# Kernel tuning notes

Measured on AMD Instinct MI355X. Metric: run time of the kernel, lower is better.

## Reference

```python
import jax, jax.numpy as jnp
import numpy as np

L, H, F, FH, MLPD = 12, 12, 768, 64, 3072  # layers, heads, d_model, head_dim, mlp hidden
GH, GW = 32, 32
N = 1 + GH * GW  # cls token + patches
EPS = 1e-6
QK_SCALE = FH ** (-0.5)
STAGE_ENDS = (2, 5, 8, 11)  # last layer index of each of the 4 stages (3 layers/stage)


def _relpos_index(h, w):
    # standard timm BEiT relative position index with 3 extra cls entries
    coords = np.stack(np.meshgrid(np.arange(h), np.arange(w), indexing="ij"))  # 2,h,w
    cf = coords.reshape(2, -1)
    rel = (cf[:, :, None] - cf[:, None, :]).transpose(1, 2, 0).astype(np.int64)  # hw,hw,2
    rel[:, :, 0] += h - 1
    rel[:, :, 1] += w - 1
    rel[:, :, 0] *= 2 * w - 1
    num_rel = (2 * h - 1) * (2 * w - 1) + 3
    idx = np.zeros((h * w + 1, h * w + 1), dtype=np.int32)
    idx[1:, 1:] = rel.sum(-1)
    idx[0, 0:] = num_rel - 3
    idx[0:, 0] = num_rel - 2
    idx[0, 0] = num_rel - 1
    return idx, num_rel


def setup_inputs() -> dict:
    key = jax.random.key(0)
    ks = jax.random.split(key, 10)
    s = 0.02
    idx, R = _relpos_index(GH, GW)
    return dict(
        patch_tokens=jax.random.normal(ks[0], (1, GH * GW, F), jnp.float32),
        cls_token=jax.random.normal(ks[1], (1, 1, F), jnp.float32) * s,
        ln1_w=jnp.ones((L, F), jnp.float32),
        ln1_b=jnp.zeros((L, F), jnp.float32),
        qkv_w=jax.random.normal(ks[2], (L, 3 * F, F), jnp.float32) * s,
        q_bias=jax.random.normal(ks[3], (L, H, FH), jnp.float32) * s,
        v_bias=jax.random.normal(ks[4], (L, H, FH), jnp.float32) * s,
        proj_w=jax.random.normal(ks[5], (L, F, F), jnp.float32) * s,
        proj_b=jnp.zeros((L, F), jnp.float32),
        scale_attn=jnp.full((L, F), 0.1, jnp.float32),
        ln2_w=jnp.ones((L, F), jnp.float32),
        ln2_b=jnp.zeros((L, F), jnp.float32),
        fc1_w=jax.random.normal(ks[6], (L, MLPD, F), jnp.float32) * s,
        fc1_b=jnp.zeros((L, MLPD), jnp.float32),
        fc2_w=jax.random.normal(ks[7], (L, F, MLPD), jnp.float32) * s,
        fc2_b=jnp.zeros((L, F), jnp.float32),
        scale_mlp=jnp.full((L, F), 0.1, jnp.float32),
        relpos_table=jax.random.normal(ks[8], (L, R, H), jnp.float32) * s,
        relpos_index=jnp.asarray(idx),
        patch_grid_hw=jnp.array([GH, GW], jnp.int32),
    )


def _ln(x, w, b):
    mu = jnp.mean(x, -1, keepdims=True)
    var = jnp.mean(jnp.square(x - mu), -1, keepdims=True)
    return (x - mu) * jax.lax.rsqrt(var + EPS) * w + b


def reference(patch_tokens, cls_token, ln1_w, ln1_b, qkv_w, q_bias, v_bias,
              proj_w, proj_b, scale_attn, ln2_w, ln2_b, fc1_w, fc1_b, fc2_w,
              fc2_b, scale_mlp, relpos_table, relpos_index, patch_grid_hw):
    B = patch_tokens.shape[0]
    tokens = jnp.concatenate(
        [jnp.broadcast_to(cls_token, (B, 1, F)), patch_tokens], axis=1)  # B,N,F

    params = dict(ln1_w=ln1_w, ln1_b=ln1_b, qkv_w=qkv_w, q_bias=q_bias,
                  v_bias=v_bias, proj_w=proj_w, proj_b=proj_b,
                  scale_attn=scale_attn, ln2_w=ln2_w, ln2_b=ln2_b,
                  fc1_w=fc1_w, fc1_b=fc1_b, fc2_w=fc2_w, fc2_b=fc2_b,
                  scale_mlp=scale_mlp, relpos_table=relpos_table)

    def step(x, p):
        h = _ln(x, p['ln1_w'], p['ln1_b'])
        qkv = jnp.einsum('bnf,gf->bng', h, p['qkv_w'])          # B,N,3F (no bias)
        qkv = qkv.reshape(B, N, 3, H, FH).transpose(2, 0, 3, 1, 4)
        q, k, v = qkv[0], qkv[1], qkv[2]                         # B,H,N,fh
        q = (q + p['q_bias'][None, :, None, :]) * QK_SCALE
        v = v + p['v_bias'][None, :, None, :]
        bias = p['relpos_table'][relpos_index]                   # N,N,H
        attn = jnp.einsum('bhnd,bhmd->bhnm', q, k) + bias.transpose(2, 0, 1)[None]
        w = jax.nn.softmax(attn, axis=-1)
        o = jnp.einsum('bhnm,bhmd->bhnd', w, v).transpose(0, 2, 1, 3).reshape(B, N, F)
        o = o @ p['proj_w'].T + p['proj_b']
        x = x + p['scale_attn'] * o
        h2 = _ln(x, p['ln2_w'], p['ln2_b'])
        m = jax.nn.gelu(h2 @ p['fc1_w'].T + p['fc1_b'], approximate=False)
        m = m @ p['fc2_w'].T + p['fc2_b']
        x = x + p['scale_mlp'] * m
        return x, x

    _, ys = jax.lax.scan(step, tokens, params)  # ys: L,B,N,F
    return (ys[STAGE_ENDS[0]], ys[STAGE_ENDS[1]], ys[STAGE_ENDS[2]], ys[STAGE_ENDS[3]])
```

## Files before the change

### kernel.cpp

```cpp
#include <hip/hip_runtime.h>
#include <hip/hip_bf16.h>
#include <math.h>

#define L_LAYERS 12
#define H_HEADS  12
#define F_DIM    768
#define FH_DIM   64
#define MLPD     3072
#define NT       1025
#define NTP      1056
#define THREE_F  2304
#define R_REL    3972
#define QK_SCALE 0.125f
#define QB       64
#define KB       128

#define CQKV  (THREE_F * F_DIM)
#define CPROJ (F_DIM * F_DIM)
#define CFC1  (MLPD * F_DIM)
#define CFC2  (F_DIM * MLPD)

typedef short short8_t __attribute__((ext_vector_type(8)));
typedef float f32x4_t  __attribute__((ext_vector_type(4)));
typedef __attribute__((address_space(1))) const void* gptr_t;
typedef __attribute__((address_space(3))) void*       lptr_t;

typedef __hip_bfloat16 bf16;

static __device__ inline unsigned short f2bf(float f) {
    __hip_bfloat16 b(f);
    unsigned short u;
    __builtin_memcpy(&u, &b, 2);
    return u;
}

__device__ inline void xcd_remap(int& tx, int& ty) {
    int gx = gridDim.x, gy = gridDim.y;
    int b = blockIdx.y * gx + blockIdx.x;
    int total = gx * gy;
    int q = total >> 3, r = total & 7;
    int xcd = b & 7, i = b >> 3;
    int pos = (xcd < r) ? xcd * (q + 1) + i : r * (q + 1) + (xcd - r) * q + i;
    ty = pos / gx;
    tx = pos - ty * gx;
}

__global__ void init_x_k(const float* __restrict__ patch, const float* __restrict__ cls,
                         float* __restrict__ x) {
    int i = blockIdx.x * 256 + threadIdx.x;
    if (i >= NT * F_DIM) return;
    int n = i / F_DIM, f = i - n * F_DIM;
    x[i] = (n == 0) ? cls[f] : patch[(size_t)(n - 1) * F_DIM + f];
}

__global__ void zero_vt_k(bf16* __restrict__ vt) {
    int i = blockIdx.x * 256 + threadIdx.x;
    int total = H_HEADS * FH_DIM * NTP;
    #pragma unroll
    for (int j = 0; j < 8; ++j) {
        int e = i * 8 + j;
        if (e < total) vt[e] = __hip_bfloat16(0.0f);
    }
}

__global__ void rp16_k(const int* __restrict__ rp, unsigned short* __restrict__ rp16) {
    int i = blockIdx.x * 256 + threadIdx.x;
    if (i < NT * NT) rp16[i] = (unsigned short)rp[i];
}

__global__ void tableT_k(const float* __restrict__ t, float* __restrict__ tt) {
    int i = blockIdx.x * 256 + threadIdx.x;
    if (i >= L_LAYERS * R_REL * H_HEADS) return;
    int l = i / (R_REL * H_HEADS), rem = i - l * (R_REL * H_HEADS);
    int rr = rem / H_HEADS, hh = rem - rr * H_HEADS;
    tt[((size_t)l * H_HEADS + hh) * R_REL + rr] = t[i];
}

__global__ void conv_all_k(const float* __restrict__ qkv_w, const float* __restrict__ proj_w,
                           const float* __restrict__ fc1_w, const float* __restrict__ fc2_w,
                           bf16* __restrict__ wq, bf16* __restrict__ wp,
                           bf16* __restrict__ w1, bf16* __restrict__ w2) {
    const long A1 = (long)L_LAYERS * CQKV;
    const long A2 = A1 + (long)L_LAYERS * CPROJ;
    const long A3 = A2 + (long)L_LAYERS * CFC1;
    const long A4 = A3 + (long)L_LAYERS * CFC2;
    const long total4 = A4 >> 2;
    for (long qd = (long)blockIdx.x * 256 + threadIdx.x; qd < total4;
         qd += (long)gridDim.x * 256) {
        long e = qd << 2;
        const float* s; bf16* d; long off;
        if (e < A1)      { s = qkv_w;  d = wq; off = e; }
        else if (e < A2) { s = proj_w; d = wp; off = e - A1; }
        else if (e < A3) { s = fc1_w;  d = w1; off = e - A2; }
        else             { s = fc2_w;  d = w2; off = e - A3; }
        float4 v = *reinterpret_cast<const float4*>(s + off);
        ushort4 o;
        o.x = f2bf(v.x); o.y = f2bf(v.y); o.z = f2bf(v.z); o.w = f2bf(v.w);
        *reinterpret_cast<ushort4*>(d + off) = o;
    }
}

__global__ void layernorm_k(const float* __restrict__ x, const float* __restrict__ w,
                            const float* __restrict__ b, bf16* __restrict__ out) {
    const int row = blockIdx.x;
    const float* xr = x + (size_t)row * F_DIM;
    float v0 = xr[threadIdx.x];
    float v1 = xr[threadIdx.x + 256];
    float v2 = xr[threadIdx.x + 512];
    float s  = v0 + v1 + v2;
    float s2 = v0 * v0 + v1 * v1 + v2 * v2;
    #pragma unroll
    for (int off = 32; off; off >>= 1) {
        s  += __shfl_down(s, off);
        s2 += __shfl_down(s2, off);
    }
    __shared__ float ws_[4], ws2_[4];
    int lane = threadIdx.x & 63, wid = threadIdx.x >> 6;
    if (lane == 0) { ws_[wid] = s; ws2_[wid] = s2; }
    __syncthreads();
    float S  = ws_[0] + ws_[1] + ws_[2] + ws_[3];
    float S2 = ws2_[0] + ws2_[1] + ws2_[2] + ws2_[3];
    float mu  = S * (1.0f / F_DIM);
    float var = S2 * (1.0f / F_DIM) - mu * mu;
    float rs  = rsqrtf(var + 1e-6f);
    bf16* orow = out + (size_t)row * F_DIM;
    orow[threadIdx.x]       = __hip_bfloat16((v0 - mu) * rs * w[threadIdx.x]       + b[threadIdx.x]);
    orow[threadIdx.x + 256] = __hip_bfloat16((v1 - mu) * rs * w[threadIdx.x + 256] + b[threadIdx.x + 256]);
    orow[threadIdx.x + 512] = __hip_bfloat16((v2 - mu) * rs * w[threadIdx.x + 512] + b[threadIdx.x + 512]);
}


template <int T, int NLOAD>
__device__ inline void stage_glds(const bf16* __restrict__ g0, int ld, int rows_rem,
                                  bf16* lds, int tid) {
    #pragma unroll
    for (int i = 0; i < NLOAD; ++i) {
        int slot = i * T + tid;
        int row = slot >> 3, s = slot & 7;
        int grow = row < rows_rem ? row : (rows_rem - 1);
        const bf16* src = g0 + (size_t)grow * ld + ((s ^ (row & 7)) * 8);
        bf16* dst = lds + (size_t)(i * T + (tid & ~63)) * 8;
        __builtin_amdgcn_global_load_lds((gptr_t)src, (lptr_t)dst, 16, 0, 0);
    }
}

template <int EPI, int BM, int BN, int WM, int WN>
__global__ __launch_bounds__((BM / (WM * 16)) * (BN / (WN * 16)) * 64)
void gemm_k(const bf16* __restrict__ A, const bf16* __restrict__ B,
            int M, int Nc, int K, int lda, int ldb,
            const float* __restrict__ p0, const float* __restrict__ p1,
            float* __restrict__ outF, float* __restrict__ outDup,
            bf16* __restrict__ outB0, bf16* __restrict__ outB1, bf16* __restrict__ outB2) {
    constexpr int NWM = BM / (WM * 16);
    constexpr int NWN = BN / (WN * 16);
    constexpr int T   = NWM * NWN * 64;
    constexpr int ALOADS = BM * 8 / T;
    constexpr int BLOADS = BN * 8 / T;

    __shared__ __align__(16) bf16 As[2][BM * 64];
    __shared__ __align__(16) bf16 Bs[2][BN * 64];

    int tx, ty;
    xcd_remap(tx, ty);
    const int tid  = threadIdx.x;
    const int lane = tid & 63, wid = tid >> 6;
    const int wr = wid / NWN, wc = wid % NWN;
    const int g4 = lane >> 4, l16 = lane & 15;
    const int bm = tx * BM, bn = ty * BN;
    const bf16* Ab = A + (size_t)bm * lda;
    const bf16* Bb = B + (size_t)bn * ldb;
    const int aRows = min(BM, M - bm);
    const int bRows = min(BN, Nc - bn);

    f32x4_t acc[WM][WN] = {};
    const int NK = K >> 6;

    stage_glds<T, ALOADS>(Ab, lda, aRows, As[0], tid);
    stage_glds<T, BLOADS>(Bb, ldb, bRows, Bs[0], tid);
    __syncthreads();

    for (int t = 0; t < NK; ++t) {
        const int c = t & 1;
        if (t + 1 < NK) {
            stage_glds<T, ALOADS>(Ab + (t + 1) * 64, lda, aRows, As[c ^ 1], tid);
            stage_glds<T, BLOADS>(Bb + (t + 1) * 64, ldb, bRows, Bs[c ^ 1], tid);
        }
        const short* AsS = reinterpret_cast<const short*>(As[c]);
        const short* BsS = reinterpret_cast<const short*>(Bs[c]);
        #pragma unroll
        for (int kk = 0; kk < 2; ++kk) {
            short8_t af[WM], bfr[WN];
            #pragma unroll
            for (int mi = 0; mi < WM; ++mi) {
                int ar = wr * WM * 16 + mi * 16 + l16;
                int j = (kk * 4 + g4) ^ (ar & 7);
                af[mi] = *reinterpret_cast<const short8_t*>(AsS + ar * 64 + j * 8);
            }
            #pragma unroll
            for (int ni = 0; ni < WN; ++ni) {
                int br = wc * WN * 16 + ni * 16 + l16;
                int j = (kk * 4 + g4) ^ (br & 7);
                bfr[ni] = *reinterpret_cast<const short8_t*>(BsS + br * 64 + j * 8);
            }
            #pragma unroll
            for (int mi = 0; mi < WM; ++mi)
                #pragma unroll
                for (int ni = 0; ni < WN; ++ni)
                    acc[mi][ni] = __builtin_amdgcn_mfma_f32_16x16x32_bf16(
                        af[mi], bfr[ni], acc[mi][ni], 0, 0, 0);
        }
        __syncthreads();
    }

    #pragma unroll
    for (int mi = 0; mi < WM; ++mi) {
        #pragma unroll
        for (int r = 0; r < 4; ++r) {
            const int row = bm + wr * WM * 16 + mi * 16 + g4 * 4 + r;
            if (row >= M) continue;
            #pragma unroll
            for (int ni = 0; ni < WN; ++ni) {
                const int col = bn + wc * WN * 16 + ni * 16 + l16;
                float v = acc[mi][ni][r];
                if (EPI == 0) {
                    if (col < F_DIM) {
                        int h = col >> 6, d = col & 63;
                        float q = (v + p0[col]) * QK_SCALE;
                        outB0[((size_t)h * NT + row) * 64 + d] = __hip_bfloat16(q);
                    } else if (col < 2 * F_DIM) {
                        int g = col - F_DIM;
                        int h = g >> 6, d = g & 63;
                        outB1[((size_t)h * NT + row) * 64 + d] = __hip_bfloat16(v);
                    } else {
                        int g = col - 2 * F_DIM;
                        int h = g >> 6, d = g & 63;
                        float vv = v + p1[g];
                        outB2[((size_t)h * 64 + d) * NTP + row] = __hip_bfloat16(vv);
                    }
                } else if (EPI == 3) {
                    size_t oi = (size_t)row * Nc + col;
                    v += p0[col];
                    float nv = outF[oi] + p1[col] * v;
                    outF[oi] = nv;
                    if (outDup) outDup[oi] = nv;
                } else if (EPI == 4) {
                    v += p0[col];
                    float g = 0.5f * v * (1.0f + erff(v * 0.70710678118654752f));
                    outB0[(size_t)row * MLPD + col] = __hip_bfloat16(g);
                }
            }
        }
    }
}

__global__ __launch_bounds__(256)
void flash_k(const bf16* __restrict__ q_bf, const bf16* __restrict__ k_bf,
             const bf16* __restrict__ v_t, const unsigned short* __restrict__ rp16,
             const float* __restrict__ tableT, bf16* __restrict__ o_bf) {
    __shared__ __align__(16) bf16 Qs[QB * 64];
    __shared__ __align__(16) bf16 Ks[2][KB * 64];
    __shared__ __align__(16) bf16 Vs[2][64 * KB];
    __shared__ __align__(16) bf16 Ps[4][16 * KB];

    int qx, h;
    xcd_remap(qx, h);
    const int tid = threadIdx.x, lane = tid & 63, w = tid >> 6;
    const int qb = qx * QB;
    const bf16* qh = q_bf + (size_t)h * NT * 64;
    const bf16* kh = k_bf + (size_t)h * NT * 64;
    const bf16* vh = v_t  + (size_t)h * 64 * NTP;
    const float* tbl = tableT + (size_t)h * R_REL;
    const int q_local = lane & 15;
    const int g4 = lane >> 4;

    auto stageKV = [&](int buf, int m0) {
        const int kRows = min(KB, NT - m0);
        #pragma unroll
        for (int i = 0; i < 4; ++i) {
            int slot = i * 256 + tid;
            int row = slot >> 3, s = slot & 7;
            int grow = min(row, kRows - 1);
            const bf16* src = kh + (size_t)(m0 + grow) * 64 + (s ^ (row & 7)) * 8;
            bf16* dst = Ks[buf] + (size_t)(i * 256 + (tid & ~63)) * 8;
            __builtin_amdgcn_global_load_lds((gptr_t)src, (lptr_t)dst, 16, 0, 0);
        }
        #pragma unroll
        for (int i = 0; i < 4; ++i) {
            int slot = i * 256 + tid;
            int d = slot >> 4, s = slot & 15;
            int msl = min(m0 / 8 + (s ^ (d & 15)), NTP / 8 - 1);
            const bf16* src = vh + (size_t)d * NTP + msl * 8;
            bf16* dst = Vs[buf] + (size_t)(i * 256 + (tid & ~63)) * 8;
            __builtin_amdgcn_global_load_lds((gptr_t)src, (lptr_t)dst, 16, 0, 0);
        }
    };

    {
        const int qRows = min(QB, NT - qb);
        #pragma unroll
        for (int i = 0; i < 2; ++i) {
            int slot = i * 256 + tid;
            int row = slot >> 3, s = slot & 7;
            int grow = min(row, qRows - 1);
            const bf16* src = qh + (size_t)(qb + grow) * 64 + (s ^ (row & 7)) * 8;
            bf16* dst = Qs + (size_t)(i * 256 + (tid & ~63)) * 8;
            __builtin_amdgcn_global_load_lds((gptr_t)src, (lptr_t)dst, 16, 0, 0);
        }
    }
    stageKV(0, 0);
    __syncthreads();

    short8_t qf[2];
    {
        const short* QsS = (const short*)Qs;
        #pragma unroll
        for (int kk = 0; kk < 2; ++kk) {
            int row = w * 16 + q_local;
            int slot = (kk * 4 + g4) ^ (row & 7);
            qf[kk] = *(const short8_t*)(QsS + row * 64 + slot * 8);
        }
    }

    float m_run[4], l_run[4];
    f32x4_t acc[4] = {};
    #pragma unroll
    for (int r = 0; r < 4; ++r) { m_run[r] = -1e30f; l_run[r] = 0.0f; }

    const int NTILES = (NT + KB - 1) / KB;
    for (int t = 0; t < NTILES; ++t) {
        const int m0 = t * KB;
        const int c = t & 1;
        if (t + 1 < NTILES) stageKV(c ^ 1, (t + 1) * KB);

        f32x4_t sfr[8];
        {
            const short* KsS = (const short*)Ks[c];
            #pragma unroll
            for (int f = 0; f < 8; ++f) {
                f32x4_t cacc = {};
                #pragma unroll
                for (int kk = 0; kk < 2; ++kk) {
                    int mrow = f * 16 + q_local;
                    int slot = (kk * 4 + g4) ^ (mrow & 7);
                    short8_t bv = *(const short8_t*)(KsS + mrow * 64 + slot * 8);
                    cacc = __builtin_amdgcn_mfma_f32_16x16x32_bf16(qf[kk], bv, cacc, 0, 0, 0);
                }
                sfr[f] = cacc;
            }
        }

        const int qrow_base = qb + w * 16 + g4 * 4;
        #pragma unroll
        for (int f = 0; f < 8; ++f) {
            int mm = m0 + f * 16 + q_local;
            if (mm < NT) {
                #pragma unroll
                for (int r = 0; r < 4; ++r) {
                    int qc = min(qrow_base + r, NT - 1);
                    int idx = rp16[(size_t)qc * NT + mm];
                    sfr[f][r] += tbl[idx];
                }
            } else {
                #pragma unroll
                for (int r = 0; r < 4; ++r) sfr[f][r] = -1e30f;
            }
        }

        float pmax[4];
        #pragma unroll
        for (int r = 0; r < 4; ++r) {
            float mx = sfr[0][r];
            #pragma unroll
            for (int f = 1; f < 8; ++f) mx = fmaxf(mx, sfr[f][r]);
            pmax[r] = mx;
        }
        #pragma unroll
        for (int off = 1; off < 16; off <<= 1)
            #pragma unroll
            for (int r = 0; r < 4; ++r) pmax[r] = fmaxf(pmax[r], __shfl_xor(pmax[r], off));

        float fac[4];
        #pragma unroll
        for (int r = 0; r < 4; ++r) {
            float mnew = fmaxf(m_run[r], pmax[r]);
            fac[r] = __expf(m_run[r] - mnew);
            m_run[r] = mnew;
        }

        float rsum[4] = {0.f, 0.f, 0.f, 0.f};
        short* PsW = (short*)Ps[w];
        #pragma unroll
        for (int f = 0; f < 8; ++f) {
            int mloc = f * 16 + q_local;
            #pragma unroll
            for (int r = 0; r < 4; ++r) {
                int ql = g4 * 4 + r;
                float p = __expf(sfr[f][r] - m_run[r]);
                rsum[r] += p;
                PsW[ql * 128 + (((mloc >> 3) ^ ql) * 8) + (mloc & 7)] = (short)f2bf(p);
            }
        }
        #pragma unroll
        for (int off = 1; off < 16; off <<= 1)
            #pragma unroll
            for (int r = 0; r < 4; ++r) rsum[r] += __shfl_xor(rsum[r], off);
        #pragma unroll
        for (int r = 0; r < 4; ++r) l_run[r] = l_run[r] * fac[r] + rsum[r];
        #pragma unroll
        for (int df = 0; df < 4; ++df)
            #pragma unroll
            for (int r = 0; r < 4; ++r) acc[df][r] *= fac[r];

        {
            const short* PsR = (const short*)Ps[w];
            const short* VsS = (const short*)Vs[c];
            #pragma unroll
            for (int kk = 0; kk < 4; ++kk) {
                int j = kk * 4 + g4;
                short8_t pa = *(const short8_t*)(PsR + q_local * 128 + (j ^ q_local) * 8);
                #pragma unroll
                for (int df = 0; df < 4; ++df) {
                    int drow = df * 16 + q_local;
                    short8_t vb = *(const short8_t*)(VsS + drow * 128 + (j ^ (drow & 15)) * 8);
                    acc[df] = __builtin_amdgcn_mfma_f32_16x16x32_bf16(pa, vb, acc[df], 0, 0, 0);
                }
            }
        }
        __syncthreads();
    }

    #pragma unroll
    for (int df = 0; df < 4; ++df) {
        #pragma unroll
        for (int r = 0; r < 4; ++r) {
            int qq = qb + w * 16 + g4 * 4 + r;
            if (qq < NT) {
                float o = acc[df][r] / l_run[r];
                o_bf[(size_t)qq * F_DIM + h * 64 + df * 16 + q_local] = __hip_bfloat16(o);
            }
        }
    }
}

extern "C" void kernel_launch(void* const* d_in, const int* in_sizes, int n_in,
                              void* d_out, int out_size, void* d_ws, size_t ws_size,
                              hipStream_t stream) {
    const float* patch      = (const float*)d_in[0];
    const float* cls        = (const float*)d_in[1];
    const float* ln1_w      = (const float*)d_in[2];
    const float* ln1_b      = (const float*)d_in[3];
    const float* qkv_w      = (const float*)d_in[4];
    const float* q_bias     = (const float*)d_in[5];
    const float* v_bias     = (const float*)d_in[6];
    const float* proj_w     = (const float*)d_in[7];
    const float* proj_b     = (const float*)d_in[8];
    const float* scale_attn = (const float*)d_in[9];
    const float* ln2_w      = (const float*)d_in[10];
    const float* ln2_b      = (const float*)d_in[11];
    const float* fc1_w      = (const float*)d_in[12];
    const float* fc1_b      = (const float*)d_in[13];
    const float* fc2_w      = (const float*)d_in[14];
    const float* fc2_b      = (const float*)d_in[15];
    const float* scale_mlp  = (const float*)d_in[16];
    const float* table      = (const float*)d_in[17];
    const int*   rp_idx     = (const int*)d_in[18];
    float* out = (float*)d_out;

    char* ws = (char*)d_ws;
    size_t off = 0;
    auto alloc = [&](size_t bytes) { char* p = ws + off; off += (bytes + 255) & ~255ULL; return p; };

    float* x      = (float*)alloc((size_t)NT * F_DIM * 4);
    bf16*  h_bf   = (bf16*) alloc((size_t)NT * F_DIM * 2);
    bf16*  q_bf   = (bf16*) alloc((size_t)H_HEADS * NT * 64 * 2);
    bf16*  k_bf   = (bf16*) alloc((size_t)H_HEADS * NT * 64 * 2);
    bf16*  v_t    = (bf16*) alloc((size_t)H_HEADS * 64 * NTP * 2);
    bf16*  o_bf   = (bf16*) alloc((size_t)NT * F_DIM * 2);
    bf16*  m1_bf  = (bf16*) alloc((size_t)NT * MLPD * 2);
    unsigned short* rp16 = (unsigned short*)alloc((size_t)NT * NT * 2);
    float* tableT = (float*)alloc((size_t)L_LAYERS * H_HEADS * R_REL * 4);
    bf16*  wq_all = (bf16*) alloc((size_t)L_LAYERS * CQKV * 2);
    bf16*  wp_all = (bf16*) alloc((size_t)L_LAYERS * CPROJ * 2);
    bf16*  w1_all = (bf16*) alloc((size_t)L_LAYERS * CFC1 * 2);
    bf16*  w2_all = (bf16*) alloc((size_t)L_LAYERS * CFC2 * 2);

    init_x_k<<<(NT * F_DIM + 255) / 256, 256, 0, stream>>>(patch, cls, x);
    zero_vt_k<<<(H_HEADS * 64 * NTP + 2047) / 2048, 256, 0, stream>>>(v_t);
    rp16_k<<<(NT * NT + 255) / 256, 256, 0, stream>>>(rp_idx, rp16);
    tableT_k<<<(L_LAYERS * R_REL * H_HEADS + 255) / 256, 256, 0, stream>>>(table, tableT);
    conv_all_k<<<2048, 256, 0, stream>>>(qkv_w, proj_w, fc1_w, fc2_w,
                                         wq_all, wp_all, w1_all, w2_all);

    int stage = 0;
    for (int l = 0; l < L_LAYERS; ++l) {
        layernorm_k<<<NT, 256, 0, stream>>>(x, ln1_w + l * F_DIM, ln1_b + l * F_DIM, h_bf);

        gemm_k<0, 64, 128, 2, 2><<<dim3(17, 18), 512, 0, stream>>>(
            h_bf, wq_all + (size_t)l * CQKV, NT, THREE_F, F_DIM, F_DIM, F_DIM,
            q_bias + (size_t)l * F_DIM, v_bias + (size_t)l * F_DIM,
            nullptr, nullptr, q_bf, k_bf, v_t);

        flash_k<<<dim3((NT + QB - 1) / QB, H_HEADS), 256, 0, stream>>>(
            q_bf, k_bf, v_t, rp16,
            tableT + (size_t)l * H_HEADS * R_REL, o_bf);

        gemm_k<3, 32, 64, 1, 2><<<dim3(33, 12), 256, 0, stream>>>(
            o_bf, wp_all + (size_t)l * CPROJ, NT, F_DIM, F_DIM, F_DIM, F_DIM,
            proj_b + (size_t)l * F_DIM, scale_attn + (size_t)l * F_DIM,
            x, nullptr, nullptr, nullptr, nullptr);

        layernorm_k<<<NT, 256, 0, stream>>>(x, ln2_w + l * F_DIM, ln2_b + l * F_DIM, h_bf);

        gemm_k<4, 64, 128, 2, 2><<<dim3(17, 24), 512, 0, stream>>>(
            h_bf, w1_all + (size_t)l * CFC1, NT, MLPD, F_DIM, F_DIM, F_DIM,
            fc1_b + (size_t)l * MLPD, nullptr,
            nullptr, nullptr, m1_bf, nullptr, nullptr);

        const bool isStage = (l == 2 || l == 5 || l == 8 || l == 11);
        float* outDup = isStage ? (out + (size_t)stage * NT * F_DIM) : nullptr;
        gemm_k<3, 32, 64, 1, 2><<<dim3(33, 12), 256, 0, stream>>>(
            m1_bf, w2_all + (size_t)l * CFC2, NT, F_DIM, MLPD, MLPD, MLPD,
            fc2_b + (size_t)l * F_DIM, scale_mlp + (size_t)l * F_DIM,
            x, outDup, nullptr, nullptr, nullptr);
        if (isStage) ++stage;
    }
}
```

Before: 1.557 ms.

## Split flash attention over KV range and add a combine kernel

The attention kernel now splits the 9 KV tiles into two halves (5 and 4) per query block and head, doubling the grid from 17x12 to 17x24 workgroups so more CUs stay busy. Each half writes unnormalized fp32 accumulators plus running max and sum to scratch, and a new combine kernel merges them with log-sum-exp rescaling into the bf16 output. The weight conversion kernel also handles 8 elements per thread with a larger grid. This adds an extra launch and fp32 scratch traffic per layer.

Result: slower. 1.934 ms (+24.2%).

```diff
diff --git a/kernel.cpp b/kernel.cpp
--- a/kernel.cpp
+++ b/kernel.cpp
@@ -14,6 +14,9 @@
 #define QK_SCALE 0.125f
 #define QB       64
 #define KB       128
+#define NKVT     9
+#define SPLIT    2
+#define TS0      5
 
 #define CQKV  (THREE_F * F_DIM)
 #define CPROJ (F_DIM * F_DIM)
@@ -84,19 +87,23 @@
     const long A2 = A1 + (long)L_LAYERS * CPROJ;
     const long A3 = A2 + (long)L_LAYERS * CFC1;
     const long A4 = A3 + (long)L_LAYERS * CFC2;
-    const long total4 = A4 >> 2;
-    for (long qd = (long)blockIdx.x * 256 + threadIdx.x; qd < total4;
-         qd += (long)gridDim.x * 256) {
-        long e = qd << 2;
+    const long total8 = A4 >> 3;
+    for (long g = (long)blockIdx.x * 256 + threadIdx.x; g < total8;
+         g += (long)gridDim.x * 256) {
+        long e = g << 3;
         const float* s; bf16* d; long off;
         if (e < A1)      { s = qkv_w;  d = wq; off = e; }
         else if (e < A2) { s = proj_w; d = wp; off = e - A1; }
         else if (e < A3) { s = fc1_w;  d = w1; off = e - A2; }
         else             { s = fc2_w;  d = w2; off = e - A3; }
-        float4 v = *reinterpret_cast<const float4*>(s + off);
-        ushort4 o;
-        o.x = f2bf(v.x); o.y = f2bf(v.y); o.z = f2bf(v.z); o.w = f2bf(v.w);
-        *reinterpret_cast<ushort4*>(d + off) = o;
+        float4 v0 = *reinterpret_cast<const float4*>(s + off);
+        float4 v1 = *reinterpret_cast<const float4*>(s + off + 4);
+        short8_t o;
+        o[0] = (short)f2bf(v0.x); o[1] = (short)f2bf(v0.y);
+        o[2] = (short)f2bf(v0.z); o[3] = (short)f2bf(v0.w);
+        o[4] = (short)f2bf(v1.x); o[5] = (short)f2bf(v1.y);
+        o[6] = (short)f2bf(v1.z); o[7] = (short)f2bf(v1.w);
+        *reinterpret_cast<short8_t*>(d + off) = o;
     }
 }
 
@@ -128,7 +135,6 @@
     orow[threadIdx.x + 256] = __hip_bfloat16((v1 - mu) * rs * w[threadIdx.x + 256] + b[threadIdx.x + 256]);
     orow[threadIdx.x + 512] = __hip_bfloat16((v2 - mu) * rs * w[threadIdx.x + 512] + b[threadIdx.x + 512]);
 }
-
 
 template <int T, int NLOAD>
 __device__ inline void stage_glds(const bf16* __restrict__ g0, int ld, int rows_rem,
@@ -256,14 +262,17 @@
 __global__ __launch_bounds__(256)
 void flash_k(const bf16* __restrict__ q_bf, const bf16* __restrict__ k_bf,
              const bf16* __restrict__ v_t, const unsigned short* __restrict__ rp16,
-             const float* __restrict__ tableT, bf16* __restrict__ o_bf) {
+             const float* __restrict__ tableT,
+             float* __restrict__ pacc, float* __restrict__ pml) {
     __shared__ __align__(16) bf16 Qs[QB * 64];
     __shared__ __align__(16) bf16 Ks[2][KB * 64];
     __shared__ __align__(16) bf16 Vs[2][64 * KB];
     __shared__ __align__(16) bf16 Ps[4][16 * KB];
 
-    int qx, h;
-    xcd_remap(qx, h);
+    int qx, yy;
+    xcd_remap(qx, yy);
+    const int h = yy >> 1, sp = yy & 1;
+    const int t0 = sp * TS0, t1 = sp ? NKVT : TS0;
     const int tid = threadIdx.x, lane = tid & 63, w = tid >> 6;
     const int qb = qx * QB;
     const bf16* qh = q_bf + (size_t)h * NT * 64;
@@ -307,7 +316,7 @@
             __builtin_amdgcn_global_load_lds((gptr_t)src, (lptr_t)dst, 16, 0, 0);
         }
     }
-    stageKV(0, 0);
+    stageKV(0, t0 * KB);
     __syncthreads();
 
     short8_t qf[2];
@@ -326,11 +335,10 @@
     #pragma unroll
     for (int r = 0; r < 4; ++r) { m_run[r] = -1e30f; l_run[r] = 0.0f; }
 
-    const int NTILES = (NT + KB - 1) / KB;
-    for (int t = 0; t < NTILES; ++t) {
+    for (int t = t0; t < t1; ++t) {
         const int m0 = t * KB;
-        const int c = t & 1;
-        if (t + 1 < NTILES) stageKV(c ^ 1, (t + 1) * KB);
+        const int c = (t - t0) & 1;
+        if (t + 1 < t1) stageKV(c ^ 1, (t + 1) * KB);
 
         f32x4_t sfr[8];
         {
@@ -435,11 +443,38 @@
         for (int r = 0; r < 4; ++r) {
             int qq = qb + w * 16 + g4 * 4 + r;
             if (qq < NT) {
-                float o = acc[df][r] / l_run[r];
-                o_bf[(size_t)qq * F_DIM + h * 64 + df * 16 + q_local] = __hip_bfloat16(o);
-            }
-        }
-    }
+                pacc[(((size_t)sp * H_HEADS + h) * NT + qq) * 64 + df * 16 + q_local] = acc[df][r];
+            }
+        }
+    }
+    if (q_local == 0) {
+        #pragma unroll
+        for (int r = 0; r < 4; ++r) {
+            int qq = qb + w * 16 + g4 * 4 + r;
+            if (qq < NT) {
+                float* st = pml + (((size_t)sp * H_HEADS + h) * NT + qq) * 2;
+                st[0] = m_run[r];
+                st[1] = l_run[r];
+            }
+        }
+    }
+}
+
+__global__ void fcomb_k(const float* __restrict__ pacc, const float* __restrict__ pml,
+                        bf16* __restrict__ o_bf) {
+    const int h = blockIdx.y;
+    const int row = blockIdx.x * 4 + (threadIdx.x >> 6);
+    const int d = threadIdx.x & 63;
+    if (row >= NT) return;
+    const size_t i0 = ((size_t)0 * H_HEADS + h) * NT + row;
+    const size_t i1 = ((size_t)1 * H_HEADS + h) * NT + row;
+    float m0 = pml[i0 * 2], l0 = pml[i0 * 2 + 1];
+    float m1 = pml[i1 * 2], l1 = pml[i1 * 2 + 1];
+    float ms = fmaxf(m0, m1);
+    float f0 = __expf(m0 - ms), f1 = __expf(m1 - ms);
+    float num = pacc[i0 * 64 + d] * f0 + pacc[i1 * 64 + d] * f1;
+    float den = l0 * f0 + l1 * f1;
+    o_bf[(size_t)row * F_DIM + h * 64 + d] = __hip_bfloat16(num / den);
 }
 
 extern "C" void kernel_launch(void* const* d_in, const int* in_sizes, int n_in,
@@ -479,6 +514,8 @@
     bf16*  m1_bf  = (bf16*) alloc((size_t)NT * MLPD * 2);
     unsigned short* rp16 = (unsigned short*)alloc((size_t)NT * NT * 2);
     float* tableT = (float*)alloc((size_t)L_LAYERS * H_HEADS * R_REL * 4);
+    float* pacc   = (float*)alloc((size_t)SPLIT * H_HEADS * NT * 64 * 4);
+    float* pml    = (float*)alloc((size_t)SPLIT * H_HEADS * NT * 2 * 4);
     bf16*  wq_all = (bf16*) alloc((size_t)L_LAYERS * CQKV * 2);
     bf16*  wp_all = (bf16*) alloc((size_t)L_LAYERS * CPROJ * 2);
     bf16*  w1_all = (bf16*) alloc((size_t)L_LAYERS * CFC1 * 2);
@@ -488,7 +525,7 @@
     zero_vt_k<<<(H_HEADS * 64 * NTP + 2047) / 2048, 256, 0, stream>>>(v_t);
     rp16_k<<<(NT * NT + 255) / 256, 256, 0, stream>>>(rp_idx, rp16);
     tableT_k<<<(L_LAYERS * R_REL * H_HEADS + 255) / 256, 256, 0, stream>>>(table, tableT);
-    conv_all_k<<<2048, 256, 0, stream>>>(qkv_w, proj_w, fc1_w, fc2_w,
+    conv_all_k<<<4096, 256, 0, stream>>>(qkv_w, proj_w, fc1_w, fc2_w,
                                          wq_all, wp_all, w1_all, w2_all);
 
     int stage = 0;
@@ -500,9 +537,10 @@
             q_bias + (size_t)l * F_DIM, v_bias + (size_t)l * F_DIM,
             nullptr, nullptr, q_bf, k_bf, v_t);
 
-        flash_k<<<dim3((NT + QB - 1) / QB, H_HEADS), 256, 0, stream>>>(
+        flash_k<<<dim3(17, H_HEADS * SPLIT), 256, 0, stream>>>(
             q_bf, k_bf, v_t, rp16,
-            tableT + (size_t)l * H_HEADS * R_REL, o_bf);
+            tableT + (size_t)l * H_HEADS * R_REL, pacc, pml);
+        fcomb_k<<<dim3((NT + 3) / 4, H_HEADS), 256, 0, stream>>>(pacc, pml, o_bf);
 
         gemm_k<3, 32, 64, 1, 2><<<dim3(33, 12), 256, 0, stream>>>(
             o_bf, wp_all + (size_t)l * CPROJ, NT, F_DIM, F_DIM, F_DIM, F_DIM,
```
